# Optimization experiments

Measured on AMD Instinct MI355X. Metric: run time of the kernel, lower is better.

The kernel has to match this reference:

```python
import jax, jax.numpy as jnp
import numpy as np

VISION_TOKEN_TYPE = 1

def _swiglu_mlp(x, w_gate, w_up, w_down):
    # x: [B, L, D]; w_gate/w_up: [D, F]; w_down: [F, D]
    g = jax.nn.silu(jnp.einsum('bld,df->blf', x, w_gate))
    u = jnp.einsum('bld,df->blf', x, w_up)
    return jnp.einsum('blf,fd->bld', g * u, w_down)

def _vision_mask(token_type_ids):
    # vision_token_mask[:, :-1] = (tt[:, :-1]==V) & (tt[:, 1:]==V); last col False
    is_v = token_type_ids == VISION_TOKEN_TYPE
    pair = is_v[:, :-1] & is_v[:, 1:]
    return jnp.concatenate([pair, jnp.zeros_like(pair[:, :1])], axis=1)  # [B, L] bool

def setup_inputs() -> dict:
    key = jax.random.key(0)
    ks = jax.random.split(key, 8)
    B, L, D, F = 2, 2048, 4096, 11008
    s = 0.02
    return {
        'hidden_states': jax.random.normal(ks[0], (B, L, D), dtype=jnp.float32),
        'token_type_ids': jax.random.randint(ks[1], (B, L), 0, 2, dtype=jnp.int64),
        'vision_gate': jax.random.normal(ks[2], (D, F), dtype=jnp.float32) * s,
        'vision_up': jax.random.normal(ks[3], (D, F), dtype=jnp.float32) * s,
        'vision_down': jax.random.normal(ks[4], (F, D), dtype=jnp.float32) * s,
        'language_gate': jax.random.normal(ks[5], (D, F), dtype=jnp.float32) * s,
        'language_up': jax.random.normal(ks[6], (D, F), dtype=jnp.float32) * s,
        'language_down': jax.random.normal(ks[7], (F, D), dtype=jnp.float32) * s,
    }

def reference(hidden_states, token_type_ids, vision_gate, vision_up, vision_down,
              language_gate, language_up, language_down):
    vmask = _vision_mask(token_type_ids)  # [B, L]
    out_v = _swiglu_mlp(hidden_states, vision_gate, vision_up, vision_down)
    out_l = _swiglu_mlp(hidden_states, language_gate, language_up, language_down)
    return jnp.where(vmask[:, :, None], out_v, out_l)
```

## Files before the change

kernel.cpp:

```cpp
#include <hip/hip_runtime.h>
#include <hip/hip_bf16.h>

#define B_    2
#define L_    2048
#define D_    4096
#define F_    11008
#define M_TOK (B_ * L_)
#define BM    256
#define M_ALLOC (M_TOK + BM)
#define NTM   (M_ALLOC / BM)
#define NT_GU (D_ / 64)
#define NT_DN (F_ / 64)
#define NTILE_F (F_ / 128)
#define SPLITK_DN 4
#define LDS_GU 131072
#define LDS_DN 131072

typedef __attribute__((ext_vector_type(8))) __bf16 bf16x8;
typedef __attribute__((ext_vector_type(4))) float  f32x4;
typedef unsigned short ushort_t;
typedef unsigned int   uint_t;


__device__ __forceinline__ void gload_lds16(const void* g, void* l) {
  __builtin_amdgcn_global_load_lds(
      (const __attribute__((address_space(1))) void*)g,
      (__attribute__((address_space(3))) void*)l, 16, 0, 0);
}

#define PH_BAR()  { __builtin_amdgcn_sched_barrier(0); __builtin_amdgcn_s_barrier(); __builtin_amdgcn_sched_barrier(0); }
#define LGKM0()   { asm volatile("s_waitcnt lgkmcnt(0)" ::: "memory"); __builtin_amdgcn_sched_barrier(0); }
#define LGKM8()   { asm volatile("s_waitcnt lgkmcnt(8)" ::: "memory"); __builtin_amdgcn_sched_barrier(0); }
#define LGKM4()   { asm volatile("s_waitcnt lgkmcnt(4)" ::: "memory"); __builtin_amdgcn_sched_barrier(0); }
#define VM4()     { asm volatile("s_waitcnt vmcnt(4)" ::: "memory"); __builtin_amdgcn_sched_barrier(0); }
#define VM0()     { asm volatile("s_waitcnt vmcnt(0)" ::: "memory"); __builtin_amdgcn_sched_barrier(0); }

__device__ __forceinline__ ushort_t f2bf(float v) {
  union { __hip_bfloat16 h; ushort_t u; } cv;
  cv.h = __float2bfloat16(v);
  return cv.u;
}

__device__ __forceinline__ int xcd_swz(int orig, int nwg) {
  const int q = nwg >> 3, r = nwg & 7, xcd = orig & 7;
  return (xcd < r ? xcd * (q + 1) : r * (q + 1) + (xcd - r) * q) + (orig >> 3);
}

__device__ __forceinline__ void stage_half(const __hip_bfloat16* __restrict__ src, int ldE,
                                           __bf16* ldsb, int w, int lane) {
#pragma unroll
  for (int j = 0; j < 2; ++j) {
    const int ch  = (w * 2 + j) * 64 + lane;
    const int row = ch >> 3;
    const int cc  = (ch & 7) ^ (row & 7);
    gload_lds16(src + (size_t)(row * ldE + cc * 8), ldsb + (w * 2 + j) * 512);
  }
}

__device__ __forceinline__ bf16x8 ldfrag(const __bf16* region, int row, int koffb) {
  const int off = ((row << 7) + koffb) ^ ((row & 7) << 4);
  return *(const bf16x8*)((const char*)region + off);
}

__device__ __forceinline__ void mfma_q(f32x4 (&acc)[8][4], int mb, int nb,
                                       const bf16x8 (&af)[4][2], const bf16x8 (&bf)[2][2]) {
#pragma unroll
  for (int mm = 0; mm < 4; ++mm)
#pragma unroll
    for (int nn = 0; nn < 2; ++nn)
#pragma unroll
      for (int ks = 0; ks < 2; ++ks)
        acc[mb + mm][nb + nn] = __builtin_amdgcn_mfma_f32_16x16x32_bf16(
            af[mm][ks], bf[nn][ks], acc[mb + mm][nb + nn], 0, 0, 0);
}

__device__ __forceinline__ void gemm_kloop(const __hip_bfloat16* __restrict__ Ag, const int ldA,
                                           const __hip_bfloat16* __restrict__ Bg, const int ldB,
                                           const int nt, __bf16* smem, f32x4 (&acc)[8][4],
                                           const int wm, const int wn, const int l15,
                                           const int l4, const int w, const int lane) {
  stage_half(Ag,             ldA, smem,                w, lane);
  stage_half(Ag + 128 * ldA, ldA, smem + 8192,         w, lane);
  stage_half(Bg,             ldB, smem + 16384,        w, lane);
  stage_half(Bg + 128 * ldB, ldB, smem + 24576,        w, lane);
  if (1 < nt) {
    stage_half(Ag + 64,             ldA, smem + 32768,        w, lane);
    stage_half(Ag + 64 + 128 * ldA, ldA, smem + 32768 + 8192, w, lane);
  }
  VM4(); PH_BAR();

  for (int t = 0; t < nt; ++t) {
    __bf16* bufc = smem + (t & 1) * 32768;
    __bf16* bufn = smem + ((t + 1) & 1) * 32768;
    const __bf16* At = bufc;
    const __bf16* Bt = bufc + 16384;
    bf16x8 a0[4][2], a1[4][2], b0[2][2], b1[2][2];

#pragma unroll
    for (int i = 0; i < 4; ++i)
#pragma unroll
      for (int ks = 0; ks < 2; ++ks)
        a0[i][ks] = ldfrag(At, wm * 128 + i * 16 + l15, ks * 64 + l4 * 16);
#pragma unroll
    for (int n = 0; n < 2; ++n)
#pragma unroll
      for (int ks = 0; ks < 2; ++ks)
        b0[n][ks] = ldfrag(Bt, wn * 64 + n * 16 + l15, ks * 64 + l4 * 16);
    if (t + 1 < nt) stage_half(Bg + (t + 1) * 64, ldB, bufn + 16384, w, lane);
    LGKM8(); PH_BAR(); LGKM0();
    __builtin_amdgcn_s_setprio(1);
    mfma_q(acc, 0, 0, a0, b0);
    __builtin_amdgcn_s_setprio(0);
    PH_BAR();

#pragma unroll
    for (int i = 0; i < 4; ++i)
#pragma unroll
      for (int ks = 0; ks < 2; ++ks)
        a1[i][ks] = ldfrag(At, wm * 128 + 64 + i * 16 + l15, ks * 64 + l4 * 16);
    if (t + 1 < nt) stage_half(Bg + (t + 1) * 64 + 128 * ldB, ldB, bufn + 24576, w, lane);
    LGKM4(); PH_BAR(); LGKM0();
    __builtin_amdgcn_s_setprio(1);
    mfma_q(acc, 4, 0, a1, b0);
    __builtin_amdgcn_s_setprio(0);
    PH_BAR();

#pragma unroll
    for (int n = 0; n < 2; ++n)
#pragma unroll
      for (int ks = 0; ks < 2; ++ks)
        b1[n][ks] = ldfrag(Bt, wn * 64 + 32 + n * 16 + l15, ks * 64 + l4 * 16);
    if (t + 2 < nt) stage_half(Ag + (t + 2) * 64, ldA, bufc, w, lane);
    PH_BAR(); LGKM0();
    __builtin_amdgcn_s_setprio(1);
    mfma_q(acc, 4, 2, a1, b1);
    __builtin_amdgcn_s_setprio(0);
    PH_BAR();

    if (t + 2 < nt) stage_half(Ag + (t + 2) * 64 + 128 * ldA, ldA, bufc + 8192, w, lane);
    __builtin_amdgcn_s_setprio(1);
    mfma_q(acc, 0, 2, a0, b1);
    __builtin_amdgcn_s_setprio(0);
    if (t + 2 < nt) { VM4(); } else { VM0(); }
    PH_BAR();
  }
}


__global__ void init_kernel(int* counters, int* slot2tok) {
  int i = blockIdx.x * 256 + threadIdx.x;
  if (i < 2) counters[i] = 0;
  if (i < M_ALLOC) slot2tok[i] = -1;
}

__global__ void assign_kernel(const int* __restrict__ tt, int* counters,
                              int* __restrict__ slot2tok) {
  int t = blockIdx.x * 256 + threadIdx.x;
  if (t >= M_TOK) return;
  int l = t & (L_ - 1);
  bool isv = (tt[t] == 1) && (l < L_ - 1) && (tt[t + 1] == 1);
  int slot;
  if (isv) slot = atomicAdd(&counters[0], 1);
  else     slot = M_ALLOC - 1 - atomicAdd(&counters[1], 1);
  slot2tok[slot] = t;
}

__global__ void gather_cvt(const float* __restrict__ x, const int* __restrict__ slot2tok,
                           __hip_bfloat16* __restrict__ xg) {
  const int s = blockIdx.x;
  const int t = slot2tok[s];
  __hip_bfloat16* dst = xg + (size_t)s * D_ + threadIdx.x * 16;
  union { ushort_t h[8]; uint4 v; } p0, p1;
  if (t >= 0) {
    const float4* s4 = (const float4*)(x + (size_t)t * D_ + threadIdx.x * 16);
    float4 a = s4[0], b = s4[1], c = s4[2], d = s4[3];
    float vals[16] = {a.x,a.y,a.z,a.w,b.x,b.y,b.z,b.w,c.x,c.y,c.z,c.w,d.x,d.y,d.z,d.w};
#pragma unroll
    for (int i = 0; i < 8; ++i) p0.h[i] = f2bf(vals[i]);
#pragma unroll
    for (int i = 0; i < 8; ++i) p1.h[i] = f2bf(vals[8 + i]);
  } else {
    p0.v = make_uint4(0, 0, 0, 0);
    p1.v = make_uint4(0, 0, 0, 0);
  }
  *(uint4*)dst = p0.v;
  *(uint4*)(dst + 8) = p1.v;
}

__global__ __launch_bounds__(128) void transpose_cvt64(const float* __restrict__ in,
                                                       __hip_bfloat16* __restrict__ out,
                                                       int R, int C) {
  const int c  = threadIdx.x & 63;
  const int rc = threadIdx.x >> 6;
  const int c0 = blockIdx.x * 64;
  const int r0 = blockIdx.y * 64 + rc * 32;
  const float* ip = in + (size_t)r0 * C + c0 + c;
  uint_t pk[16];
#pragma unroll
  for (int j = 0; j < 16; ++j) {
    float v0 = ip[(size_t)(2 * j) * C];
    float v1 = ip[(size_t)(2 * j + 1) * C];
    pk[j] = (uint_t)f2bf(v0) | ((uint_t)f2bf(v1) << 16);
  }
  uint4* op = (uint4*)(out + (size_t)(c0 + c) * R + r0);
#pragma unroll
  for (int k = 0; k < 4; ++k)
    op[k] = make_uint4(pk[4 * k], pk[4 * k + 1], pk[4 * k + 2], pk[4 * k + 3]);
}

__global__ void sentinel_kernel(float* out, int n) {
  int i = blockIdx.x * 256 + threadIdx.x;
  if (i < n) out[i] = 1e30f;
}

__global__ __launch_bounds__(512, 2) void gemm256_gateup_fused(
    const __hip_bfloat16* __restrict__ Xg,
    const __hip_bfloat16* __restrict__ WgTv, const __hip_bfloat16* __restrict__ WuTv,
    const __hip_bfloat16* __restrict__ WgTl, const __hip_bfloat16* __restrict__ WuTl,
    __hip_bfloat16* __restrict__ H, const int* __restrict__ counters) {
  extern __shared__ __bf16 smem[];
  const int tid = threadIdx.x, lane = tid & 63, w = tid >> 6;
  const int wm = w >> 1, wn = w & 1;
  const int l15 = lane & 15, l4 = lane >> 4;

  const int wg = xcd_swz(blockIdx.x, gridDim.x);
  const int mt = wg % NTM, ntile = wg / NTM;
  const int row0 = mt * BM;
  const int ncol0 = ntile * 128;
  const int nv = counters[0];
  const bool isv = row0 < nv;
  const __hip_bfloat16* Ag   = Xg + (size_t)row0 * D_;
  const __hip_bfloat16* Bg_g = (isv ? WgTv : WgTl) + (size_t)ncol0 * D_;
  const __hip_bfloat16* Bu_g = (isv ? WuTv : WuTl) + (size_t)ncol0 * D_;

  f32x4 accg[4][4] = {};
  f32x4 accu[4][4] = {};
  const int nt = NT_GU;

  stage_half(Ag,                  D_, smem,          w, lane);
  stage_half(Ag + 128 * D_,       D_, smem + 8192,   w, lane);
  stage_half(Bg_g,                D_, smem + 32768,  w, lane);
  stage_half(Bu_g,                D_, smem + 49152,  w, lane);
  stage_half(Ag + 64,             D_, smem + 16384,  w, lane);
  stage_half(Ag + 64 + 128 * D_,  D_, smem + 24576,  w, lane);
  VM4(); PH_BAR();

  for (int t = 0; t < nt; ++t) {
    const int cur = t & 1;
    const __bf16* At  = smem + cur * 16384;
    const __bf16* Bgt = smem + 32768 + cur * 8192;
    const __bf16* But = smem + 49152 + cur * 8192;
    __bf16* nxA  = smem + cur * 16384;
    __bf16* nxBg = smem + 32768 + (cur ^ 1) * 8192;
    __bf16* nxBu = smem + 49152 + (cur ^ 1) * 8192;
    bf16x8 af[4][2], bb[4][2];

#pragma unroll
    for (int m = 0; m < 2; ++m)
#pragma unroll
      for (int ks = 0; ks < 2; ++ks)
        af[m][ks] = ldfrag(At, wm * 64 + m * 16 + l15, ks * 64 + l4 * 16);
#pragma unroll
    for (int n = 0; n < 4; ++n)
#pragma unroll
      for (int ks = 0; ks < 2; ++ks)
        bb[n][ks] = ldfrag(Bgt, wn * 64 + n * 16 + l15, ks * 64 + l4 * 16);
    if (t + 1 < nt) stage_half(Bg_g + (t + 1) * 64, D_, nxBg, w, lane);
    LGKM8(); PH_BAR(); LGKM0();
    __builtin_amdgcn_s_setprio(1);
#pragma unroll
    for (int m = 0; m < 2; ++m)
#pragma unroll
      for (int n = 0; n < 4; ++n)
#pragma unroll
        for (int ks = 0; ks < 2; ++ks)
          accg[m][n] = __builtin_amdgcn_mfma_f32_16x16x32_bf16(
              af[m][ks], bb[n][ks], accg[m][n], 0, 0, 0);
    __builtin_amdgcn_s_setprio(0);
    PH_BAR();

#pragma unroll
    for (int m = 2; m < 4; ++m)
#pragma unroll
      for (int ks = 0; ks < 2; ++ks)
        af[m][ks] = ldfrag(At, wm * 64 + m * 16 + l15, ks * 64 + l4 * 16);
    if (t + 1 < nt) stage_half(Bu_g + (t + 1) * 64, D_, nxBu, w, lane);
    PH_BAR(); LGKM0();
    __builtin_amdgcn_s_setprio(1);
#pragma unroll
    for (int m = 2; m < 4; ++m)
#pragma unroll
      for (int n = 0; n < 4; ++n)
#pragma unroll
        for (int ks = 0; ks < 2; ++ks)
          accg[m][n] = __builtin_amdgcn_mfma_f32_16x16x32_bf16(
              af[m][ks], bb[n][ks], accg[m][n], 0, 0, 0);
    __builtin_amdgcn_s_setprio(0);
    PH_BAR();

#pragma unroll
    for (int n = 0; n < 4; ++n)
#pragma unroll
      for (int ks = 0; ks < 2; ++ks)
        bb[n][ks] = ldfrag(But, wn * 64 + n * 16 + l15, ks * 64 + l4 * 16);
    if (t + 2 < nt) stage_half(Ag + (t + 2) * 64, D_, nxA, w, lane);
    LGKM4(); PH_BAR(); LGKM0();
    __builtin_amdgcn_s_setprio(1);
#pragma unroll
    for (int m = 0; m < 2; ++m)
#pragma unroll
      for (int n = 0; n < 4; ++n)
#pragma unroll
        for (int ks = 0; ks < 2; ++ks)
          accu[m][n] = __builtin_amdgcn_mfma_f32_16x16x32_bf16(
              af[m][ks], bb[n][ks], accu[m][n], 0, 0, 0);
    __builtin_amdgcn_s_setprio(0);
    PH_BAR();

    if (t + 2 < nt) stage_half(Ag + (t + 2) * 64 + 128 * D_, D_, nxA + 8192, w, lane);
    __builtin_amdgcn_s_setprio(1);
#pragma unroll
    for (int m = 2; m < 4; ++m)
#pragma unroll
      for (int n = 0; n < 4; ++n)
#pragma unroll
        for (int ks = 0; ks < 2; ++ks)
          accu[m][n] = __builtin_amdgcn_mfma_f32_16x16x32_bf16(
              af[m][ks], bb[n][ks], accu[m][n], 0, 0, 0);
    __builtin_amdgcn_s_setprio(0);
    if (t + 2 < nt) { VM4(); } else { VM0(); }
    PH_BAR();
  }

#pragma unroll
  for (int m = 0; m < 4; ++m) {
    const int grow = row0 + wm * 64 + m * 16 + l4 * 4;
#pragma unroll
    for (int rr = 0; rr < 4; ++rr) {
      __hip_bfloat16* orow = H + (size_t)(grow + rr) * F_ + ncol0 + wn * 64 + l15;
#pragma unroll
      for (int n = 0; n < 4; ++n) {
        const float g = accg[m][n][rr];
        const float u = accu[m][n][rr];
        orow[n * 16] = __float2bfloat16(g / (1.0f + __expf(-g)) * u);
      }
    }
  }
}


__global__ __launch_bounds__(512, 2) void gemm256_down(
    const __hip_bfloat16* __restrict__ H,
    const __hip_bfloat16* __restrict__ WdTv, const __hip_bfloat16* __restrict__ WdTl,
    float* __restrict__ out, const int* __restrict__ counters,
    const int* __restrict__ slot2tok) {
  extern __shared__ __bf16 smem[];
  const int tid = threadIdx.x, lane = tid & 63, w = tid >> 6;
  const int wm = w >> 2, wn = w & 3;
  const int l15 = lane & 15, l4 = lane >> 4;

  const int wg = xcd_swz(blockIdx.x, gridDim.x);
  const int mt = wg % NTM, ntt = wg / NTM;
  const int z  = blockIdx.y;
  const int row0 = mt * BM;
  const int ncol0 = ntt * 256;
  const int ntz = NT_DN / SPLITK_DN;
  const int t0 = z * ntz;
  const int nv = counters[0];
  const __hip_bfloat16* Bsrc = (row0 < nv) ? WdTv : WdTl;
  const __hip_bfloat16* Ag = H + (size_t)row0 * F_ + t0 * 64;
  const __hip_bfloat16* Bg = Bsrc + (size_t)ncol0 * F_ + t0 * 64;

  f32x4 acc[8][4] = {};
  gemm_kloop(Ag, F_, Bg, F_, ntz, smem, acc, wm, wn, l15, l4, w, lane);

#pragma unroll
  for (int m = 0; m < 8; ++m) {
    const int slot = row0 + wm * 128 + m * 16 + l4 * 4;
#pragma unroll
    for (int rr = 0; rr < 4; ++rr) {
      const int tok = slot2tok[slot + rr];
      if (tok < 0) continue;
      float* orow = out + (size_t)tok * D_ + ncol0 + wn * 64 + l15;
#pragma unroll
      for (int n = 0; n < 4; ++n)
        atomicAdd(&orow[n * 16], acc[m][n][rr]);
    }
  }
}


extern "C" void kernel_launch(void* const* d_in, const int* in_sizes, int n_in,
                              void* d_out, int out_size, void* d_ws, size_t ws_size,
                              hipStream_t stream) {
  const float* x   = (const float*)d_in[0];
  const int*   tt  = (const int*)d_in[1];
  const float* wgv = (const float*)d_in[2];
  const float* wuv = (const float*)d_in[3];
  const float* wdv = (const float*)d_in[4];
  const float* wgl = (const float*)d_in[5];
  const float* wul = (const float*)d_in[6];
  const float* wdl = (const float*)d_in[7];
  float* out = (float*)d_out;

  size_t off = 0;
  auto nalign = [](size_t v) { return (v + 255) & ~(size_t)255; };
  const size_t o_cnt = off; off += nalign(2 * sizeof(int));
  const size_t o_s2t = off; off += nalign((size_t)M_ALLOC * sizeof(int));
  const size_t o_xg  = off; off += nalign((size_t)M_ALLOC * D_ * 2);
  const size_t o_h   = off; off += nalign((size_t)M_ALLOC * F_ * 2);
  const size_t wbytes = nalign((size_t)D_ * F_ * 2);
  const size_t o_wgv = off; off += wbytes;
  const size_t o_wuv = off; off += wbytes;
  const size_t o_wgl = off; off += wbytes;
  const size_t o_wul = off; off += wbytes;

  if (ws_size < off) {
    sentinel_kernel<<<(out_size + 255) / 256, 256, 0, stream>>>(out, out_size);
    return;
  }

  char* ws = (char*)d_ws;
  int* counters = (int*)(ws + o_cnt);
  int* slot2tok = (int*)(ws + o_s2t);
  __hip_bfloat16* Xg  = (__hip_bfloat16*)(ws + o_xg);
  __hip_bfloat16* H   = (__hip_bfloat16*)(ws + o_h);
  __hip_bfloat16* WgTv = (__hip_bfloat16*)(ws + o_wgv);
  __hip_bfloat16* WuTv = (__hip_bfloat16*)(ws + o_wuv);
  __hip_bfloat16* WgTl = (__hip_bfloat16*)(ws + o_wgl);
  __hip_bfloat16* WuTl = (__hip_bfloat16*)(ws + o_wul);
  __hip_bfloat16* WdTv = WgTv;
  __hip_bfloat16* WdTl = WuTv;

  hipFuncSetAttribute((const void*)gemm256_gateup_fused,
                      hipFuncAttributeMaxDynamicSharedMemorySize, LDS_GU);
  hipFuncSetAttribute((const void*)gemm256_down,
                      hipFuncAttributeMaxDynamicSharedMemorySize, LDS_DN);

  hipMemsetAsync(out, 0, (size_t)out_size * sizeof(float), stream);

  init_kernel<<<(M_ALLOC + 255) / 256, 256, 0, stream>>>(counters, slot2tok);
  assign_kernel<<<(M_TOK + 255) / 256, 256, 0, stream>>>(tt, counters, slot2tok);
  gather_cvt<<<M_ALLOC, 256, 0, stream>>>(x, slot2tok, Xg);

  dim3 tb(128);
  dim3 tg_gu(F_ / 64, D_ / 64);
  transpose_cvt64<<<tg_gu, tb, 0, stream>>>(wgv, WgTv, D_, F_);
  transpose_cvt64<<<tg_gu, tb, 0, stream>>>(wuv, WuTv, D_, F_);
  transpose_cvt64<<<tg_gu, tb, 0, stream>>>(wgl, WgTl, D_, F_);
  transpose_cvt64<<<tg_gu, tb, 0, stream>>>(wul, WuTl, D_, F_);

  gemm256_gateup_fused<<<dim3(NTM * NTILE_F), 512, LDS_GU, stream>>>(
      Xg, WgTv, WuTv, WgTl, WuTl, H, counters);

  dim3 tg_dn(D_ / 64, F_ / 64);
  transpose_cvt64<<<tg_dn, tb, 0, stream>>>(wdv, WdTv, F_, D_);
  transpose_cvt64<<<tg_dn, tb, 0, stream>>>(wdl, WdTl, F_, D_);

  gemm256_down<<<dim3(NTM * (D_ / 256), SPLITK_DN), 512, LDS_DN, stream>>>(
      H, WdTv, WdTl, out, counters, slot2tok);
}
```

Baseline: 1.640 ms.

## Prefetch B tiles two stages ahead and batch weight transpose launches

Both GEMM k-loops now stage A and B tiles two iterations ahead, replacing the earlier scheme where B was fetched only one step ahead. The prologue loads two full stages and waits with vmcnt(8), and the per-phase lgkm partial waits are removed. This gives global loads more time to land before they are consumed, at the cost of more loads in flight and a changed LDS buffer layout. The separate weight transpose/convert launches are also merged into batched kernels that pick their source by blockIdx.y, cutting launch count.

```diff
diff --git a/kernel.cpp b/kernel.cpp
--- a/kernel.cpp
+++ b/kernel.cpp
@@ -30,9 +30,7 @@
 
 #define PH_BAR()  { __builtin_amdgcn_sched_barrier(0); __builtin_amdgcn_s_barrier(); __builtin_amdgcn_sched_barrier(0); }
 #define LGKM0()   { asm volatile("s_waitcnt lgkmcnt(0)" ::: "memory"); __builtin_amdgcn_sched_barrier(0); }
-#define LGKM8()   { asm volatile("s_waitcnt lgkmcnt(8)" ::: "memory"); __builtin_amdgcn_sched_barrier(0); }
-#define LGKM4()   { asm volatile("s_waitcnt lgkmcnt(4)" ::: "memory"); __builtin_amdgcn_sched_barrier(0); }
-#define VM4()     { asm volatile("s_waitcnt vmcnt(4)" ::: "memory"); __builtin_amdgcn_sched_barrier(0); }
+#define VM8()     { asm volatile("s_waitcnt vmcnt(8)" ::: "memory"); __builtin_amdgcn_sched_barrier(0); }
 #define VM0()     { asm volatile("s_waitcnt vmcnt(0)" ::: "memory"); __builtin_amdgcn_sched_barrier(0); }
 
 __device__ __forceinline__ ushort_t f2bf(float v) {
@@ -79,21 +77,23 @@
                                            const int nt, __bf16* smem, f32x4 (&acc)[8][4],
                                            const int wm, const int wn, const int l15,
                                            const int l4, const int w, const int lane) {
-  stage_half(Ag,             ldA, smem,                w, lane);
-  stage_half(Ag + 128 * ldA, ldA, smem + 8192,         w, lane);
-  stage_half(Bg,             ldB, smem + 16384,        w, lane);
-  stage_half(Bg + 128 * ldB, ldB, smem + 24576,        w, lane);
-  if (1 < nt) {
-    stage_half(Ag + 64,             ldA, smem + 32768,        w, lane);
-    stage_half(Ag + 64 + 128 * ldA, ldA, smem + 32768 + 8192, w, lane);
-  }
-  VM4(); PH_BAR();
+  stage_half(Ag,                  ldA, smem,          w, lane);
+  stage_half(Ag + 128 * ldA,      ldA, smem + 8192,   w, lane);
+  stage_half(Bg,                  ldB, smem + 32768,  w, lane);
+  stage_half(Bg + 128 * ldB,      ldB, smem + 40960,  w, lane);
+  stage_half(Ag + 64,             ldA, smem + 16384,  w, lane);
+  stage_half(Ag + 64 + 128 * ldA, ldA, smem + 24576,  w, lane);
+  stage_half(Bg + 64,             ldB, smem + 49152,  w, lane);
+  stage_half(Bg + 64 + 128 * ldB, ldB, smem + 57344,  w, lane);
+  VM8(); PH_BAR();
 
   for (int t = 0; t < nt; ++t) {
-    __bf16* bufc = smem + (t & 1) * 32768;
-    __bf16* bufn = smem + ((t + 1) & 1) * 32768;
-    const __bf16* At = bufc;
-    const __bf16* Bt = bufc + 16384;
+    const int cur = t & 1;
+    const __bf16* At = smem + cur * 16384;
+    const __bf16* Bt = smem + 32768 + cur * 16384;
+    __bf16* nxA = smem + cur * 16384;
+    __bf16* nxB = smem + 32768 + cur * 16384;
+    const bool s2 = (t + 2 < nt);
     bf16x8 a0[4][2], a1[4][2], b0[2][2], b1[2][2];
 
 #pragma unroll
@@ -106,8 +106,7 @@
 #pragma unroll
       for (int ks = 0; ks < 2; ++ks)
         b0[n][ks] = ldfrag(Bt, wn * 64 + n * 16 + l15, ks * 64 + l4 * 16);
-    if (t + 1 < nt) stage_half(Bg + (t + 1) * 64, ldB, bufn + 16384, w, lane);
-    LGKM8(); PH_BAR(); LGKM0();
+    PH_BAR(); LGKM0();
     __builtin_amdgcn_s_setprio(1);
     mfma_q(acc, 0, 0, a0, b0);
     __builtin_amdgcn_s_setprio(0);
@@ -118,8 +117,7 @@
 #pragma unroll
       for (int ks = 0; ks < 2; ++ks)
         a1[i][ks] = ldfrag(At, wm * 128 + 64 + i * 16 + l15, ks * 64 + l4 * 16);
-    if (t + 1 < nt) stage_half(Bg + (t + 1) * 64 + 128 * ldB, ldB, bufn + 24576, w, lane);
-    LGKM4(); PH_BAR(); LGKM0();
+    PH_BAR(); LGKM0();
     __builtin_amdgcn_s_setprio(1);
     mfma_q(acc, 4, 0, a1, b0);
     __builtin_amdgcn_s_setprio(0);
@@ -130,18 +128,24 @@
 #pragma unroll
       for (int ks = 0; ks < 2; ++ks)
         b1[n][ks] = ldfrag(Bt, wn * 64 + 32 + n * 16 + l15, ks * 64 + l4 * 16);
-    if (t + 2 < nt) stage_half(Ag + (t + 2) * 64, ldA, bufc, w, lane);
+    if (s2) {
+      stage_half(Ag + (t + 2) * 64,            ldA, nxA,        w, lane);
+      stage_half(Ag + (t + 2) * 64 + 128 * ldA, ldA, nxA + 8192, w, lane);
+    }
     PH_BAR(); LGKM0();
     __builtin_amdgcn_s_setprio(1);
     mfma_q(acc, 4, 2, a1, b1);
     __builtin_amdgcn_s_setprio(0);
     PH_BAR();
 
-    if (t + 2 < nt) stage_half(Ag + (t + 2) * 64 + 128 * ldA, ldA, bufc + 8192, w, lane);
+    if (s2) {
+      stage_half(Bg + (t + 2) * 64,            ldB, nxB,        w, lane);
+      stage_half(Bg + (t + 2) * 64 + 128 * ldB, ldB, nxB + 8192, w, lane);
+    }
     __builtin_amdgcn_s_setprio(1);
     mfma_q(acc, 0, 2, a0, b1);
     __builtin_amdgcn_s_setprio(0);
-    if (t + 2 < nt) { VM4(); } else { VM0(); }
+    if (s2) { VM8(); } else { VM0(); }
     PH_BAR();
   }
 }
@@ -187,13 +191,24 @@
   *(uint4*)(dst + 8) = p1.v;
 }
 
-__global__ __launch_bounds__(128) void transpose_cvt64(const float* __restrict__ in,
-                                                       __hip_bfloat16* __restrict__ out,
-                                                       int R, int C) {
+__global__ __launch_bounds__(128) void transpose_cvt64_b4(
+    const float* __restrict__ s0, const float* __restrict__ s1,
+    const float* __restrict__ s2, const float* __restrict__ s3,
+    __hip_bfloat16* __restrict__ d0, __hip_bfloat16* __restrict__ d1,
+    __hip_bfloat16* __restrict__ d2, __hip_bfloat16* __restrict__ d3,
+    int R, int C) {
+  const float* in;
+  __hip_bfloat16* out;
+  switch (blockIdx.y) {
+    case 0:  in = s0; out = d0; break;
+    case 1:  in = s1; out = d1; break;
+    case 2:  in = s2; out = d2; break;
+    default: in = s3; out = d3; break;
+  }
+  const int cb = C >> 6;
+  const int c0 = (blockIdx.x % cb) * 64;
+  const int r0 = (blockIdx.x / cb) * 64 + (threadIdx.x >> 6) * 32;
   const int c  = threadIdx.x & 63;
-  const int rc = threadIdx.x >> 6;
-  const int c0 = blockIdx.x * 64;
-  const int r0 = blockIdx.y * 64 + rc * 32;
   const float* ip = in + (size_t)r0 * C + c0 + c;
   uint_t pk[16];
 #pragma unroll
@@ -243,7 +258,9 @@
   stage_half(Bu_g,                D_, smem + 49152,  w, lane);
   stage_half(Ag + 64,             D_, smem + 16384,  w, lane);
   stage_half(Ag + 64 + 128 * D_,  D_, smem + 24576,  w, lane);
-  VM4(); PH_BAR();
+  stage_half(Bg_g + 64,           D_, smem + 40960,  w, lane);
+  stage_half(Bu_g + 64,           D_, smem + 57344,  w, lane);
+  VM8(); PH_BAR();
 
   for (int t = 0; t < nt; ++t) {
     const int cur = t & 1;
@@ -251,8 +268,9 @@
     const __bf16* Bgt = smem + 32768 + cur * 8192;
     const __bf16* But = smem + 49152 + cur * 8192;
     __bf16* nxA  = smem + cur * 16384;
-    __bf16* nxBg = smem + 32768 + (cur ^ 1) * 8192;
-    __bf16* nxBu = smem + 49152 + (cur ^ 1) * 8192;
+    __bf16* nxBg = smem + 32768 + cur * 8192;
+    __bf16* nxBu = smem + 49152 + cur * 8192;
+    const bool s2 = (t + 2 < nt);
     bf16x8 af[4][2], bb[4][2];
 
 #pragma unroll
@@ -265,8 +283,7 @@
 #pragma unroll
       for (int ks = 0; ks < 2; ++ks)
         bb[n][ks] = ldfrag(Bgt, wn * 64 + n * 16 + l15, ks * 64 + l4 * 16);
-    if (t + 1 < nt) stage_half(Bg_g + (t + 1) * 64, D_, nxBg, w, lane);
-    LGKM8(); PH_BAR(); LGKM0();
+    PH_BAR(); LGKM0();
     __builtin_amdgcn_s_setprio(1);
 #pragma unroll
     for (int m = 0; m < 2; ++m)
@@ -284,7 +301,6 @@
 #pragma unroll
       for (int ks = 0; ks < 2; ++ks)
         af[m][ks] = ldfrag(At, wm * 64 + m * 16 + l15, ks * 64 + l4 * 16);
-    if (t + 1 < nt) stage_half(Bu_g + (t + 1) * 64, D_, nxBu, w, lane);
     PH_BAR(); LGKM0();
     __builtin_amdgcn_s_setprio(1);
 #pragma unroll
@@ -303,8 +319,11 @@
 #pragma unroll
       for (int ks = 0; ks < 2; ++ks)
         bb[n][ks] = ldfrag(But, wn * 64 + n * 16 + l15, ks * 64 + l4 * 16);
-    if (t + 2 < nt) stage_half(Ag + (t + 2) * 64, D_, nxA, w, lane);
-    LGKM4(); PH_BAR(); LGKM0();
+    if (s2) {
+      stage_half(Ag + (t + 2) * 64,            D_, nxA,        w, lane);
+      stage_half(Ag + (t + 2) * 64 + 128 * D_, D_, nxA + 8192, w, lane);
+    }
+    PH_BAR(); LGKM0();
     __builtin_amdgcn_s_setprio(1);
 #pragma unroll
     for (int m = 0; m < 2; ++m)
@@ -317,7 +336,10 @@
     __builtin_amdgcn_s_setprio(0);
     PH_BAR();
 
-    if (t + 2 < nt) stage_half(Ag + (t + 2) * 64 + 128 * D_, D_, nxA + 8192, w, lane);
+    if (s2) {
+      stage_half(Bg_g + (t + 2) * 64, D_, nxBg, w, lane);
+      stage_half(Bu_g + (t + 2) * 64, D_, nxBu, w, lane);
+    }
     __builtin_amdgcn_s_setprio(1);
 #pragma unroll
     for (int m = 2; m < 4; ++m)
@@ -328,7 +350,7 @@
           accu[m][n] = __builtin_amdgcn_mfma_f32_16x16x32_bf16(
               af[m][ks], bb[n][ks], accu[m][n], 0, 0, 0);
     __builtin_amdgcn_s_setprio(0);
-    if (t + 2 < nt) { VM4(); } else { VM0(); }
+    if (s2) { VM8(); } else { VM0(); }
     PH_BAR();
   }
 
@@ -444,18 +466,15 @@
   gather_cvt<<<M_ALLOC, 256, 0, stream>>>(x, slot2tok, Xg);
 
   dim3 tb(128);
-  dim3 tg_gu(F_ / 64, D_ / 64);
-  transpose_cvt64<<<tg_gu, tb, 0, stream>>>(wgv, WgTv, D_, F_);
-  transpose_cvt64<<<tg_gu, tb, 0, stream>>>(wuv, WuTv, D_, F_);
-  transpose_cvt64<<<tg_gu, tb, 0, stream>>>(wgl, WgTl, D_, F_);
-  transpose_cvt64<<<tg_gu, tb, 0, stream>>>(wul, WuTl, D_, F_);
+  const int tblocks = (F_ / 64) * (D_ / 64);
+  transpose_cvt64_b4<<<dim3(tblocks, 4), tb, 0, stream>>>(
+      wgv, wuv, wgl, wul, WgTv, WuTv, WgTl, WuTl, D_, F_);
 
   gemm256_gateup_fused<<<dim3(NTM * NTILE_F), 512, LDS_GU, stream>>>(
       Xg, WgTv, WuTv, WgTl, WuTl, H, counters);
 
-  dim3 tg_dn(D_ / 64, F_ / 64);
-  transpose_cvt64<<<tg_dn, tb, 0, stream>>>(wdv, WdTv, F_, D_);
-  transpose_cvt64<<<tg_dn, tb, 0, stream>>>(wdl, WdTl, F_, D_);
+  transpose_cvt64_b4<<<dim3(tblocks, 2), tb, 0, stream>>>(
+      wdv, wdl, wdv, wdl, WdTv, WdTl, WdTv, WdTl, F_, D_);
 
   gemm256_down<<<dim3(NTM * (D_ / 256), SPLITK_DN), 512, LDS_DN, stream>>>(
       H, WdTv, WdTl, out, counters, slot2tok);
```

Result: slower. 1.692 ms (+3.2%).
